# Kernel tuning notes

Measured on AMD Instinct MI355X. Metric: run time of the kernel, lower is better.

The kernel has to match this reference:

```python
import jax, jax.numpy as jnp
import numpy as np
from jax import lax

BETA = 0.9
SLOPE = 25.0
THRESHOLD = 1.0
TIME_STEPS = 50


@jax.custom_vjp
def spike_fn(mem):
    # Heaviside fire: spk = 1 if mem > threshold
    return (mem > THRESHOLD).astype(mem.dtype)

def _spike_fwd(mem):
    return spike_fn(mem), mem

def _spike_bwd(mem, g):
    # snntorch fast_sigmoid surrogate: grad = 1 / (slope*|mem - thr| + 1)^2
    denom = SLOPE * jnp.abs(mem - THRESHOLD) + 1.0
    return (g / (denom * denom),)

spike_fn.defvjp(_spike_fwd, _spike_bwd)


def setup_inputs() -> dict:
    key = jax.random.key(0)
    k = jax.random.split(key, 5)
    B, D, H, O = 16384, 784, 128, 10
    return {
        "data": jax.random.normal(k[0], (B, D), dtype=jnp.float32),
        "W1": jax.random.normal(k[1], (H, D), dtype=jnp.float32) * (1.0 / np.sqrt(D)),
        "b1": jax.random.normal(k[2], (H,), dtype=jnp.float32) * 0.01,
        "W2": jax.random.normal(k[3], (O, H), dtype=jnp.float32) * (1.0 / np.sqrt(H)),
        "b2": jax.random.normal(k[4], (O,), dtype=jnp.float32) * 0.01,
    }


def reference(data, W1, b1, W2, b2):
    B = data.shape[0]
    H, O = W1.shape[0], W2.shape[0]
    # Input current to layer 1 is constant across time steps (static image).
    cur1 = data @ W1.T + b1  # [B, H]

    def step(carry, _):
        mem1, mem2 = carry
        # snntorch Leaky (reset_mechanism='subtract'):
        #   reset = detach(spk(mem_t)); mem_{t+1} = beta*mem_t + I - reset*thr; spk = fire(mem_{t+1})
        rst1 = lax.stop_gradient((mem1 > THRESHOLD).astype(mem1.dtype))
        mem1 = BETA * mem1 + cur1 - rst1 * THRESHOLD
        spk1 = spike_fn(mem1)

        cur2 = spk1 @ W2.T + b2  # [B, O]
        rst2 = lax.stop_gradient((mem2 > THRESHOLD).astype(mem2.dtype))
        mem2 = BETA * mem2 + cur2 - rst2 * THRESHOLD
        spk2 = spike_fn(mem2)
        return (mem1, mem2), spk2

    init = (jnp.zeros((B, H), data.dtype), jnp.zeros((B, O), data.dtype))
    _, spk_rec = lax.scan(step, init, None, length=TIME_STEPS)
    return spk_rec  # [time_steps, B, 10]
```

## Files before the change

kernel.cpp:

```cpp
#include <hip/hip_runtime.h>


#define TSTEPS 50
#define NB 16384
#define ND 784
#define NH 128
#define NO 10

__global__ void w1_transpose(const float* __restrict__ W1, float* __restrict__ Wt)
{
    const int k = blockIdx.x;
    const int n = threadIdx.x;
    Wt[k * NH + n] = W1[n * ND + k];
}

__global__ __launch_bounds__(256)
void gemm_cur1(const float* __restrict__ data, const float* __restrict__ Wt,
               const float* __restrict__ b1, float* __restrict__ cur1)
{
    const int tid  = threadIdx.x;
    const int bm   = blockIdx.x >> 1;
    const int bn   = blockIdx.x & 1;
    const int row0 = bm * 64;
    const int col0 = bn * 64;
    const int ty   = tid >> 4;
    const int tn   = tid & 15;

    const float* aP0 = data + (size_t)(row0 + ty * 4 + 0) * ND;
    const float* aP1 = data + (size_t)(row0 + ty * 4 + 1) * ND;
    const float* aP2 = data + (size_t)(row0 + ty * 4 + 2) * ND;
    const float* aP3 = data + (size_t)(row0 + ty * 4 + 3) * ND;
    const float* bP  = Wt + col0 + tn * 4;

    float acc[4][4] = {};

    float4 aCur[4], bCur[4];
    aCur[0] = *(const float4*)(aP0);
    aCur[1] = *(const float4*)(aP1);
    aCur[2] = *(const float4*)(aP2);
    aCur[3] = *(const float4*)(aP3);
    bCur[0] = *(const float4*)(bP + 0 * NH);
    bCur[1] = *(const float4*)(bP + 1 * NH);
    bCur[2] = *(const float4*)(bP + 2 * NH);
    bCur[3] = *(const float4*)(bP + 3 * NH);

    for (int c = 0; c < 196; ++c) {
        float4 aNxt[4], bNxt[4];
        if (c < 195) {
            const int k4 = (c + 1) * 4;
            aNxt[0] = *(const float4*)(aP0 + k4);
            aNxt[1] = *(const float4*)(aP1 + k4);
            aNxt[2] = *(const float4*)(aP2 + k4);
            aNxt[3] = *(const float4*)(aP3 + k4);
            bNxt[0] = *(const float4*)(bP + (size_t)(k4 + 0) * NH);
            bNxt[1] = *(const float4*)(bP + (size_t)(k4 + 1) * NH);
            bNxt[2] = *(const float4*)(bP + (size_t)(k4 + 2) * NH);
            bNxt[3] = *(const float4*)(bP + (size_t)(k4 + 3) * NH);
        }
        #pragma unroll
        for (int kk = 0; kk < 4; ++kk) {
            float a[4] = { ((const float*)&aCur[0])[kk],
                           ((const float*)&aCur[1])[kk],
                           ((const float*)&aCur[2])[kk],
                           ((const float*)&aCur[3])[kk] };
            float b[4] = { ((const float*)&bCur[kk])[0],
                           ((const float*)&bCur[kk])[1],
                           ((const float*)&bCur[kk])[2],
                           ((const float*)&bCur[kk])[3] };
            #pragma unroll
            for (int i = 0; i < 4; ++i)
                #pragma unroll
                for (int j = 0; j < 4; ++j)
                    acc[i][j] = fmaf(a[i], b[j], acc[i][j]);
        }
        #pragma unroll
        for (int q = 0; q < 4; ++q) { aCur[q] = aNxt[q]; bCur[q] = bNxt[q]; }
    }

    float4 bv1 = *(const float4*)&b1[col0 + tn * 4];
    #pragma unroll
    for (int i = 0; i < 4; ++i) {
        float4 o;
        o.x = acc[i][0] + bv1.x;
        o.y = acc[i][1] + bv1.y;
        o.z = acc[i][2] + bv1.z;
        o.w = acc[i][3] + bv1.w;
        *(float4*)&cur1[(size_t)(row0 + ty * 4 + i) * NH + col0 + tn * 4] = o;
    }
}

__device__ __forceinline__ float xmove_dpp_b1(float v) {
    return __int_as_float(__builtin_amdgcn_update_dpp(
        0, __float_as_int(v), 0xB1, 0xF, 0xF, true));
}
__device__ __forceinline__ float xmove_dpp_b2(float v) {
    return __int_as_float(__builtin_amdgcn_update_dpp(
        0, __float_as_int(v), 0x4E, 0xF, 0xF, true));
}
__device__ __forceinline__ float xmove_dpp_b8(float v) {
    return __int_as_float(__builtin_amdgcn_update_dpp(
        0, __float_as_int(v), 0x128, 0xF, 0xF, true));
}
__device__ __forceinline__ float xmove_swz_b4(float v) {
    return __int_as_float(__builtin_amdgcn_ds_swizzle(
        __float_as_int(v), 0x101F));
}

__global__ void snn_loop(const float* __restrict__ cur1,
                         const float* __restrict__ W2,
                         const float* __restrict__ b2,
                         float* __restrict__ out)
{
    const int tid = threadIdx.x;
    const int hg  = tid & 15;
    const int rl  = tid >> 4;
    const int row = blockIdx.x * 16 + rl;
    const int h0  = hg * 8;

    float w2[10][8];
    #pragma unroll
    for (int o = 0; o < 10; ++o) {
        float4 u = *(const float4*)&W2[o * NH + h0];
        float4 v = *(const float4*)&W2[o * NH + h0 + 4];
        w2[o][0] = u.x; w2[o][1] = u.y; w2[o][2] = u.z; w2[o][3] = u.w;
        w2[o][4] = v.x; w2[o][5] = v.y; w2[o][6] = v.z; w2[o][7] = v.w;
    }
    const float b2r = b2[hg < 10 ? hg : 0];

    float c[8];
    {
        float4 c0 = *(const float4*)&cur1[(size_t)row * NH + h0];
        float4 c1 = *(const float4*)&cur1[(size_t)row * NH + h0 + 4];
        c[0] = c0.x; c[1] = c0.y; c[2] = c0.z; c[3] = c0.w;
        c[4] = c1.x; c[5] = c1.y; c[6] = c1.z; c[7] = c1.w;
    }

    float mem1[8], spk1[8];
    #pragma unroll
    for (int j = 0; j < 8; ++j) { mem1[j] = 0.f; spk1[j] = 0.f; }
    float mem2 = 0.f, spk2 = 0.f;

    for (int t = 0; t < TSTEPS; ++t) {
        #pragma unroll
        for (int j = 0; j < 8; ++j) {
            float m = __fadd_rn(__fmul_rn(0.9f, mem1[j]), c[j]);
            m = __fsub_rn(m, spk1[j]);
            mem1[j] = m;
            spk1[j] = (m > 1.0f) ? 1.0f : 0.0f;
        }
        float p[10];
        #pragma unroll
        for (int o = 0; o < 10; ++o) p[o] = 0.f;
        #pragma unroll
        for (int j = 0; j < 8; ++j)
            #pragma unroll
            for (int o = 0; o < 10; ++o)
                p[o] = fmaf(spk1[j], w2[o][j], p[o]);
        #pragma unroll
        for (int o = 0; o < 10; ++o) p[o] += xmove_dpp_b1(p[o]);
        #pragma unroll
        for (int o = 0; o < 10; ++o) p[o] += xmove_dpp_b2(p[o]);
        #pragma unroll
        for (int o = 0; o < 10; ++o) p[o] += xmove_swz_b4(p[o]);
        #pragma unroll
        for (int o = 0; o < 10; ++o) p[o] += xmove_dpp_b8(p[o]);
        float tot = p[0];
        #pragma unroll
        for (int o = 1; o < 10; ++o)
            tot = (hg == o) ? p[o] : tot;
        float cur2 = __fadd_rn(tot, b2r);
        float m2 = __fsub_rn(__fadd_rn(__fmul_rn(0.9f, mem2), cur2), spk2);
        mem2 = m2;
        spk2 = (m2 > 1.0f) ? 1.0f : 0.0f;
        if (hg < 10)
            out[(size_t)t * (NB * NO) + row * NO + hg] = spk2;
    }
}

extern "C" void kernel_launch(void* const* d_in, const int* in_sizes, int n_in,
                              void* d_out, int out_size, void* d_ws, size_t ws_size,
                              hipStream_t stream) {
    const float* data = (const float*)d_in[0];
    const float* W1   = (const float*)d_in[1];
    const float* b1   = (const float*)d_in[2];
    const float* W2   = (const float*)d_in[3];
    const float* b2   = (const float*)d_in[4];
    float* out  = (float*)d_out;

    float* cur1 = (float*)d_ws;
    float* Wt   = (float*)((char*)d_ws + (size_t)NB * NH * 4);

    w1_transpose<<<ND, NH, 0, stream>>>(W1, Wt);
    gemm_cur1<<<512, 256, 0, stream>>>(data, Wt, b1, cur1);
    snn_loop<<<1024, 256, 0, stream>>>(cur1, W2, b2, out);
}
```

Baseline: 252.4 us.

## Pack W1 into per-thread 4x4 tiles and double-buffer GEMM loads two chunks ahead

Repacks the transposed W1 so each thread's 4x4 B sub-tile for a k-chunk sits in 16 contiguous floats, turning four strided loads into four consecutive float4 loads. The GEMM loop now keeps two register buffers and prefetches two k-chunks ahead, so global loads have more time to complete before the FMAs that use them. This raises register pressure in gemm_cur1 and changes the packing kernel's launch shape.

Result: slower. 276.3 us (+9.5%).

```diff
diff --git a/kernel.cpp b/kernel.cpp
--- a/kernel.cpp
+++ b/kernel.cpp
@@ -7,15 +7,21 @@
 #define NH 128
 #define NO 10
 
-__global__ void w1_transpose(const float* __restrict__ W1, float* __restrict__ Wt)
+__global__ void w1_pack(const float* __restrict__ W1, float* __restrict__ Wt4)
 {
-    const int k = blockIdx.x;
-    const int n = threadIdx.x;
-    Wt[k * NH + n] = W1[n * ND + k];
+    const int e = blockIdx.x * 256 + threadIdx.x;
+    if (e >= 196 * 32 * 16) return;
+    const int r  = e & 15;
+    const int g  = e >> 4;
+    const int i  = r >> 2;
+    const int j  = r & 3;
+    const int kc = g >> 5;
+    const int ng = g & 31;
+    Wt4[e] = W1[(size_t)(ng * 4 + j) * ND + kc * 4 + i];
 }
 
 __global__ __launch_bounds__(256)
-void gemm_cur1(const float* __restrict__ data, const float* __restrict__ Wt,
+void gemm_cur1(const float* __restrict__ data, const float* __restrict__ Wt4,
                const float* __restrict__ b1, float* __restrict__ cur1)
 {
     const int tid  = threadIdx.x;
@@ -30,52 +36,65 @@
     const float* aP1 = data + (size_t)(row0 + ty * 4 + 1) * ND;
     const float* aP2 = data + (size_t)(row0 + ty * 4 + 2) * ND;
     const float* aP3 = data + (size_t)(row0 + ty * 4 + 3) * ND;
-    const float* bP  = Wt + col0 + tn * 4;
+    const float* bP  = Wt4 + (size_t)(bn * 16 + tn) * 16;
 
     float acc[4][4] = {};
 
-    float4 aCur[4], bCur[4];
-    aCur[0] = *(const float4*)(aP0);
-    aCur[1] = *(const float4*)(aP1);
-    aCur[2] = *(const float4*)(aP2);
-    aCur[3] = *(const float4*)(aP3);
-    bCur[0] = *(const float4*)(bP + 0 * NH);
-    bCur[1] = *(const float4*)(bP + 1 * NH);
-    bCur[2] = *(const float4*)(bP + 2 * NH);
-    bCur[3] = *(const float4*)(bP + 3 * NH);
-
-    for (int c = 0; c < 196; ++c) {
-        float4 aNxt[4], bNxt[4];
-        if (c < 195) {
-            const int k4 = (c + 1) * 4;
-            aNxt[0] = *(const float4*)(aP0 + k4);
-            aNxt[1] = *(const float4*)(aP1 + k4);
-            aNxt[2] = *(const float4*)(aP2 + k4);
-            aNxt[3] = *(const float4*)(aP3 + k4);
-            bNxt[0] = *(const float4*)(bP + (size_t)(k4 + 0) * NH);
-            bNxt[1] = *(const float4*)(bP + (size_t)(k4 + 1) * NH);
-            bNxt[2] = *(const float4*)(bP + (size_t)(k4 + 2) * NH);
-            bNxt[3] = *(const float4*)(bP + (size_t)(k4 + 3) * NH);
-        }
-        #pragma unroll
-        for (int kk = 0; kk < 4; ++kk) {
-            float a[4] = { ((const float*)&aCur[0])[kk],
-                           ((const float*)&aCur[1])[kk],
-                           ((const float*)&aCur[2])[kk],
-                           ((const float*)&aCur[3])[kk] };
-            float b[4] = { ((const float*)&bCur[kk])[0],
-                           ((const float*)&bCur[kk])[1],
-                           ((const float*)&bCur[kk])[2],
-                           ((const float*)&bCur[kk])[3] };
-            #pragma unroll
-            for (int i = 0; i < 4; ++i)
-                #pragma unroll
-                for (int j = 0; j < 4; ++j)
-                    acc[i][j] = fmaf(a[i], b[j], acc[i][j]);
-        }
-        #pragma unroll
-        for (int q = 0; q < 4; ++q) { aCur[q] = aNxt[q]; bCur[q] = bNxt[q]; }
-    }
+    float4 aQ[2][4], bQ[2][4];
+    #pragma unroll
+    for (int s = 0; s < 2; ++s) {
+        const int k4 = s * 4;
+        aQ[s][0] = *(const float4*)(aP0 + k4);
+        aQ[s][1] = *(const float4*)(aP1 + k4);
+        aQ[s][2] = *(const float4*)(aP2 + k4);
+        aQ[s][3] = *(const float4*)(aP3 + k4);
+        const float* bc = bP + (size_t)s * 512;
+        bQ[s][0] = *(const float4*)(bc);
+        bQ[s][1] = *(const float4*)(bc + 4);
+        bQ[s][2] = *(const float4*)(bc + 8);
+        bQ[s][3] = *(const float4*)(bc + 12);
+    }
+
+    #define DO_CHUNK(s, c)                                                    \
+    {                                                                         \
+        float a[4][4], b[4][4];                                               \
+        _Pragma("unroll")                                                     \
+        for (int r = 0; r < 4; ++r) {                                         \
+            a[r][0] = aQ[s][r].x; a[r][1] = aQ[s][r].y;                       \
+            a[r][2] = aQ[s][r].z; a[r][3] = aQ[s][r].w;                       \
+        }                                                                     \
+        _Pragma("unroll")                                                     \
+        for (int i = 0; i < 4; ++i) {                                         \
+            b[i][0] = bQ[s][i].x; b[i][1] = bQ[s][i].y;                       \
+            b[i][2] = bQ[s][i].z; b[i][3] = bQ[s][i].w;                       \
+        }                                                                     \
+        if ((c) + 2 < 196) {                \
+            const int k4 = ((c) + 2) * 4;                                     \
+            aQ[s][0] = *(const float4*)(aP0 + k4);                            \
+            aQ[s][1] = *(const float4*)(aP1 + k4);                            \
+            aQ[s][2] = *(const float4*)(aP2 + k4);                            \
+            aQ[s][3] = *(const float4*)(aP3 + k4);                            \
+            const float* bc = bP + (size_t)((c) + 2) * 512;                   \
+            bQ[s][0] = *(const float4*)(bc);                                  \
+            bQ[s][1] = *(const float4*)(bc + 4);                              \
+            bQ[s][2] = *(const float4*)(bc + 8);                              \
+            bQ[s][3] = *(const float4*)(bc + 12);                             \
+        }                                                                     \
+                                     \
+        _Pragma("unroll")                                                     \
+        for (int kk = 0; kk < 4; ++kk)                                        \
+            _Pragma("unroll")                                                 \
+            for (int i = 0; i < 4; ++i)                                       \
+                _Pragma("unroll")                                             \
+                for (int j = 0; j < 4; ++j)                                   \
+                    acc[i][j] = fmaf(a[i][kk], b[kk][j], acc[i][j]);          \
+    }
+
+    for (int cc = 0; cc < 98; ++cc) {
+        DO_CHUNK(0, 2 * cc);
+        DO_CHUNK(1, 2 * cc + 1);
+    }
+    #undef DO_CHUNK
 
     float4 bv1 = *(const float4*)&b1[col0 + tn * 4];
     #pragma unroll
@@ -188,9 +207,9 @@
     float* out  = (float*)d_out;
 
     float* cur1 = (float*)d_ws;
-    float* Wt   = (float*)((char*)d_ws + (size_t)NB * NH * 4);
-
-    w1_transpose<<<ND, NH, 0, stream>>>(W1, Wt);
-    gemm_cur1<<<512, 256, 0, stream>>>(data, Wt, b1, cur1);
+    float* Wt4  = (float*)((char*)d_ws + (size_t)NB * NH * 4);
+
+    w1_pack<<<392, 256, 0, stream>>>(W1, Wt4);
+    gemm_cur1<<<512, 256, 0, stream>>>(data, Wt4, b1, cur1);
     snn_loop<<<1024, 256, 0, stream>>>(cur1, W2, b2, out);
 }
```
